# Performance work log

Hardware: AMD Instinct MI355X
Metric: run time of the kernel (lower is better)

## Reference

```python
import jax, jax.numpy as jnp
import numpy as np

N_NODES = 50000
N_EDGES = 800000
IN_DIM = 256
OUT_DIM = 32
NUM_HEADS = 8


def setup_inputs() -> dict:
    key = jax.random.key(0)
    ks = jax.random.split(key, 9)
    h = jax.random.normal(ks[0], (N_NODES, IN_DIM), dtype=jnp.float32)
    src = jax.random.randint(ks[1], (N_EDGES,), 0, N_NODES, dtype=jnp.int32)
    dst = jax.random.randint(ks[2], (N_EDGES,), 0, N_NODES, dtype=jnp.int32)
    s = 1.0 / np.sqrt(IN_DIM)
    W_lin = jax.random.uniform(ks[3], (IN_DIM, IN_DIM), jnp.float32, -s, s)
    b_lin = jax.random.uniform(ks[4], (IN_DIM,), jnp.float32, -s, s)
    # DGL GATConv fc: Linear(in_feats, out_feats*num_heads, bias=False)
    W_gat = jax.random.normal(ks[5], (IN_DIM, NUM_HEADS * OUT_DIM), dtype=jnp.float32) * s
    attn_l = jax.random.normal(ks[6], (NUM_HEADS, OUT_DIM), dtype=jnp.float32) * 0.1
    attn_r = jax.random.normal(ks[7], (NUM_HEADS, OUT_DIM), dtype=jnp.float32) * 0.1
    gat_bias = jnp.zeros((NUM_HEADS * OUT_DIM,), dtype=jnp.float32)
    return {"h": h, "src": src, "dst": dst, "W_lin": W_lin, "b_lin": b_lin,
            "W_gat": W_gat, "attn_l": attn_l, "attn_r": attn_r, "gat_bias": gat_bias}


def reference(h, src, dst, W_lin, b_lin, W_gat, attn_l, attn_r, gat_bias):
    N = h.shape[0]
    # pre-linear (nn.Linear(in_dim, in_dim))
    h = h @ W_lin + b_lin                                   # [N, in_dim]
    h_in = h
    # GATConv (eval mode: feat_drop/attn_drop are identity)
    feat = (h @ W_gat).reshape(N, NUM_HEADS, OUT_DIM)       # [N, H, D]
    el = jnp.sum(feat * attn_l, axis=-1)                    # [N, H]
    er = jnp.sum(feat * attn_r, axis=-1)                    # [N, H]
    e = jax.nn.leaky_relu(el[src] + er[dst], 0.2)           # [E, H]  (DGL slope 0.2)
    # edge softmax normalized over incoming edges of each dst node
    m = jax.ops.segment_max(e, dst, num_segments=N)         # [N, H]
    m = jnp.where(jnp.isfinite(m), m, 0.0)                  # guard empty segments
    e = jnp.exp(e - m[dst])                                 # [E, H]
    s = jax.ops.segment_sum(e, dst, num_segments=N)         # [N, H]
    a = e / s[dst]                                          # [E, H]
    # weighted neighbor aggregation
    msg = feat[src] * a[:, :, None]                         # [E, H, D]
    out = jax.ops.segment_sum(msg, dst, num_segments=N)     # [N, H, D]
    out = out.reshape(N, NUM_HEADS * OUT_DIM) + gat_bias
    # GATLayer activation: F.leaky_relu (default slope 0.01), then residual
    out = jax.nn.leaky_relu(out, 0.01)
    return h_in + out
```

## Files before the change

kernel.cpp:

```cpp
#include <hip/hip_runtime.h>
#include <math.h>

#define NN 50000
#define NE 800000
#define DIM 256
#define NH 8
#define HD 32
#define CAP 64
#define GEMM_GRID ((NN + 63) / 64)
#define SCAT_GRID ((NE / 4 + 255) / 256)

typedef __attribute__((ext_vector_type(8))) short bf16x8;
typedef __attribute__((ext_vector_type(4))) float f32x4;
typedef unsigned short u16;

__device__ __forceinline__ u16 f2bf(float f) {
    unsigned u = __float_as_uint(f);
    return (u16)((u + 0x7FFFu + ((u >> 16) & 1u)) >> 16);
}

__global__ __launch_bounds__(256) void k_pack_zero(
    const float* __restrict__ Wl, const float* __restrict__ Wg,
    u16* __restrict__ Bl, u16* __restrict__ Bg, int* __restrict__ deg)
{
    int b = blockIdx.x;
    if (b < 512) {
        const float* W = (b < 256) ? Wl : Wg;
        u16* Bp = (b < 256) ? Bl : Bg;
        int idx = (b & 255) * 256 + threadIdx.x;
        int j    = idx & 7;
        int lane = (idx >> 3) & 63;
        int ks   = (idx >> 9) & 7;
        int nf   = idx >> 12;
        int n = nf * 16 + (lane & 15);
        int k = ks * 32 + (lane >> 4) * 8 + j;
        Bp[idx] = f2bf(W[k * 256 + n]);
    } else {
        int i = (b - 512) * 256 + threadIdx.x;
        if (i < NN / 4)
            ((int4*)deg)[i] = (int4){0, 0, 0, 0};
    }
}

template<int AF32, int DO_ELER, int HAS_BIAS>
__device__ void gemm_body(int bid, const void* __restrict__ A,
    const u16* __restrict__ Bp, const float* __restrict__ bias,
    u16* __restrict__ Cb, const float* __restrict__ attn_l,
    const float* __restrict__ attn_r, float* __restrict__ el,
    float* __restrict__ er, int M, u16* Bs)
{
    const int t    = threadIdx.x;
    const int lane = t & 63;
    const int wid  = t >> 6;
    const int row0 = bid * 64 + wid * 16;
    const int arow = min(row0 + (lane & 15), M - 1);
    const int kgrp = lane >> 4;

    bf16x8 af[8];
    if (AF32) {
        const float* ap = (const float*)A + (size_t)arow * DIM + kgrp * 8;
        #pragma unroll
        for (int ks = 0; ks < 8; ++ks) {
            float4 x = *(const float4*)(ap + ks * 32);
            float4 y = *(const float4*)(ap + ks * 32 + 4);
            bf16x8 v;
            v[0] = (short)f2bf(x.x); v[1] = (short)f2bf(x.y);
            v[2] = (short)f2bf(x.z); v[3] = (short)f2bf(x.w);
            v[4] = (short)f2bf(y.x); v[5] = (short)f2bf(y.y);
            v[6] = (short)f2bf(y.z); v[7] = (short)f2bf(y.w);
            af[ks] = v;
        }
    } else {
        const u16* ap = (const u16*)A + (size_t)arow * DIM + kgrp * 8;
        #pragma unroll
        for (int ks = 0; ks < 8; ++ks)
            af[ks] = *(const bf16x8*)(ap + ks * 32);
    }

    const int crow0 = row0 + (lane >> 4) * 4;
    const int ccol  = lane & 15;

    uint4 v0, v1, v2, v3;
    {
        const uint4* p = (const uint4*)Bp + t;
        v0 = p[0]; v1 = p[256]; v2 = p[512]; v3 = p[768];
    }

    for (int c = 0; c < 8; ++c) {
        __syncthreads();
        {
            uint4* q = (uint4*)Bs + t;
            q[0] = v0; q[256] = v1; q[512] = v2; q[768] = v3;
        }
        if (c < 7) {
            const uint4* p = (const uint4*)(Bp + (size_t)(c + 1) * 8192) + t;
            v0 = p[0]; v1 = p[256]; v2 = p[512]; v3 = p[768];
        }
        __syncthreads();

        f32x4 acc0 = (f32x4){0.f, 0.f, 0.f, 0.f};
        f32x4 acc1 = (f32x4){0.f, 0.f, 0.f, 0.f};
        const u16* ls = Bs + lane * 8;
        #pragma unroll
        for (int ks = 0; ks < 8; ++ks) {
            bf16x8 b0 = *(const bf16x8*)(ls + (size_t)ks * 512);
            bf16x8 b1 = *(const bf16x8*)(ls + (size_t)(8 + ks) * 512);
            acc0 = __builtin_amdgcn_mfma_f32_16x16x32_bf16(af[ks], b0, acc0, 0, 0, 0);
            acc1 = __builtin_amdgcn_mfma_f32_16x16x32_bf16(af[ks], b1, acc1, 0, 0, 0);
        }

        {
            int col0 = c * 32 + ccol;
            int col1 = col0 + 16;
            float bv0 = HAS_BIAS ? bias[col0] : 0.f;
            float bv1 = HAS_BIAS ? bias[col1] : 0.f;
            #pragma unroll
            for (int r = 0; r < 4; ++r) {
                int row = crow0 + r;
                if (row < M) {
                    Cb[(size_t)row * DIM + col0] = f2bf(acc0[r] + bv0);
                    Cb[(size_t)row * DIM + col1] = f2bf(acc1[r] + bv1);
                }
            }
        }

        if (DO_ELER) {
            float al0 = attn_l[c * HD + ccol], al1 = attn_l[c * HD + ccol + 16];
            float ar0 = attn_r[c * HD + ccol], ar1 = attn_r[c * HD + ccol + 16];
            float ep[4], rp[4];
            #pragma unroll
            for (int r = 0; r < 4; ++r) {
                ep[r] = acc0[r] * al0 + acc1[r] * al1;
                rp[r] = acc0[r] * ar0 + acc1[r] * ar1;
            }
            #pragma unroll
            for (int off = 1; off < 16; off <<= 1) {
                #pragma unroll
                for (int r = 0; r < 4; ++r) {
                    ep[r] += __shfl_xor(ep[r], off, 64);
                    rp[r] += __shfl_xor(rp[r], off, 64);
                }
            }
            int rsel = ccol & 3;
            float ev = (rsel == 0) ? ep[0] : (rsel == 1) ? ep[1] : (rsel == 2) ? ep[2] : ep[3];
            float rv = (rsel == 0) ? rp[0] : (rsel == 1) ? rp[1] : (rsel == 2) ? rp[2] : rp[3];
            int row = crow0 + rsel;
            if (ccol < 4)      { if (row < M) el[(size_t)row * NH + c] = ev; }
            else if (ccol < 8) { if (row < M) er[(size_t)row * NH + c] = rv; }
        }
    }
}

__global__ __launch_bounds__(256) void k_gemm1_scatter(
    const float* __restrict__ h, const u16* __restrict__ Bp1,
    const float* __restrict__ b_lin, u16* __restrict__ h1b,
    const int* __restrict__ src, const int* __restrict__ dst,
    int* __restrict__ deg, int* __restrict__ csr_pad)
{
    __shared__ u16 Bs[8192];
    int bid = blockIdx.x;
    if (bid < GEMM_GRID) {
        gemm_body<1, 0, 1>(bid, h, Bp1, b_lin, h1b,
                           nullptr, nullptr, nullptr, nullptr, NN, Bs);
    } else {
        int e0 = ((bid - GEMM_GRID) * 256 + threadIdx.x) * 4;
        if (e0 >= NE) return;
        int4 sv = *(const int4*)(src + e0);
        int4 dv = *(const int4*)(dst + e0);
        int p;
        p = atomicAdd(&deg[dv.x], 1); if (p < CAP) csr_pad[dv.x * CAP + p] = sv.x;
        p = atomicAdd(&deg[dv.y], 1); if (p < CAP) csr_pad[dv.y * CAP + p] = sv.y;
        p = atomicAdd(&deg[dv.z], 1); if (p < CAP) csr_pad[dv.z * CAP + p] = sv.z;
        p = atomicAdd(&deg[dv.w], 1); if (p < CAP) csr_pad[dv.w * CAP + p] = sv.w;
    }
}

__global__ __launch_bounds__(256) void k_gemm2(
    const u16* __restrict__ h1b, const u16* __restrict__ Bp2,
    u16* __restrict__ featb, const float* __restrict__ attn_l,
    const float* __restrict__ attn_r, float* __restrict__ el,
    float* __restrict__ er)
{
    __shared__ u16 Bs[8192];
    gemm_body<0, 1, 0>(blockIdx.x, h1b, Bp2, nullptr, featb,
                       attn_l, attn_r, el, er, NN, Bs);
}

#define BODYR(j)                                                         \
    {                                                                    \
        int   s  = __shfl(s_l, base32 + j0 + (j), 64);                   \
        float wv = __shfl((j) < 4 ? w0 : w1,                             \
                          base32 + ((j) & 3) * 8 + myhead, 64);          \
        uint4 fv = *(const uint4*)(featb + (size_t)s * DIM + c);         \
        acc0 += __uint_as_float(fv.x << 16)         * wv;                \
        acc1 += __uint_as_float(fv.x & 0xFFFF0000u) * wv;                \
        acc2 += __uint_as_float(fv.y << 16)         * wv;                \
        acc3 += __uint_as_float(fv.y & 0xFFFF0000u) * wv;                \
        acc4 += __uint_as_float(fv.z << 16)         * wv;                \
        acc5 += __uint_as_float(fv.z & 0xFFFF0000u) * wv;                \
        acc6 += __uint_as_float(fv.w << 16)         * wv;                \
        acc7 += __uint_as_float(fv.w & 0xFFFF0000u) * wv;                \
        sw   += wv;                                                      \
    }

__global__ __launch_bounds__(256) void aggregate_hw(
    const int* __restrict__ deg, const int* __restrict__ csr_pad,
    const float* __restrict__ el, const float* __restrict__ er,
    const u16* __restrict__ featb, const u16* __restrict__ h1b,
    const float* __restrict__ bias, float* __restrict__ out)
{
    const int t      = threadIdx.x;
    const int hl     = t & 31;
    const int d      = blockIdx.x * 8 + (t >> 5);
    const int myhead = hl >> 2;
    const int c      = hl * 8;
    const int base32 = t & 32;
    const int cnt  = min(deg[d], CAP);
    const int* ebase = csr_pad + (size_t)d * CAP;
    const float er_p = er[(size_t)d * NH + (hl & 7)];

    float acc0 = 0.f, acc1 = 0.f, acc2 = 0.f, acc3 = 0.f;
    float acc4 = 0.f, acc5 = 0.f, acc6 = 0.f, acc7 = 0.f, sw = 0.f;

    for (int base = 0; base < cnt; base += 32) {
        const int nb = min(32, cnt - base);
        int s_l = (hl < nb) ? ebase[base + hl] : 0;
        for (int j0 = 0; j0 < nb; j0 += 8) {
            const int m = min(8, nb - j0);
            int e0 = min(j0 + (hl >> 3), nb - 1);
            int e1 = min(j0 + 4 + (hl >> 3), nb - 1);
            int se0 = __shfl(s_l, base32 + e0, 64);
            int se1 = __shfl(s_l, base32 + e1, 64);
            float x0 = el[(size_t)se0 * NH + (hl & 7)] + er_p;
            float x1 = el[(size_t)se1 * NH + (hl & 7)] + er_p;
            x0 = x0 > 0.f ? x0 : 0.2f * x0;
            x1 = x1 > 0.f ? x1 : 0.2f * x1;
            float w0 = __expf(x0);
            float w1 = __expf(x1);
            if (m == 8) {
                int ss[8];
                #pragma unroll
                for (int j = 0; j < 8; ++j) ss[j] = __shfl(s_l, base32 + j0 + j, 64);
                uint4 fv[8];
                #pragma unroll
                for (int j = 0; j < 8; ++j)
                    fv[j] = *(const uint4*)(featb + (size_t)ss[j] * DIM + c);
                __builtin_amdgcn_sched_barrier(0);
                #pragma unroll
                for (int j = 0; j < 8; ++j) {
                    float wv = __shfl(j < 4 ? w0 : w1,
                                      base32 + (j & 3) * 8 + myhead, 64);
                    acc0 += __uint_as_float(fv[j].x << 16)         * wv;
                    acc1 += __uint_as_float(fv[j].x & 0xFFFF0000u) * wv;
                    acc2 += __uint_as_float(fv[j].y << 16)         * wv;
                    acc3 += __uint_as_float(fv[j].y & 0xFFFF0000u) * wv;
                    acc4 += __uint_as_float(fv[j].z << 16)         * wv;
                    acc5 += __uint_as_float(fv[j].z & 0xFFFF0000u) * wv;
                    acc6 += __uint_as_float(fv[j].w << 16)         * wv;
                    acc7 += __uint_as_float(fv[j].w & 0xFFFF0000u) * wv;
                    sw   += wv;
                }
            } else {
                for (int j = 0; j < m; ++j) BODYR(j)
            }
        }
    }

    const float rs = (cnt > 0) ? 1.f / sw : 0.f;
    uint4  hv = *(const uint4*)(h1b + (size_t)d * DIM + c);
    float4 b0 = *(const float4*)(bias + c);
    float4 b1 = *(const float4*)(bias + c + 4);
    float r;
    float4 o0, o1;
    r = acc0 * rs + b0.x; r = r > 0.f ? r : 0.01f * r; o0.x = __uint_as_float(hv.x << 16)         + r;
    r = acc1 * rs + b0.y; r = r > 0.f ? r : 0.01f * r; o0.y = __uint_as_float(hv.x & 0xFFFF0000u) + r;
    r = acc2 * rs + b0.z; r = r > 0.f ? r : 0.01f * r; o0.z = __uint_as_float(hv.y << 16)         + r;
    r = acc3 * rs + b0.w; r = r > 0.f ? r : 0.01f * r; o0.w = __uint_as_float(hv.y & 0xFFFF0000u) + r;
    r = acc4 * rs + b1.x; r = r > 0.f ? r : 0.01f * r; o1.x = __uint_as_float(hv.z << 16)         + r;
    r = acc5 * rs + b1.y; r = r > 0.f ? r : 0.01f * r; o1.y = __uint_as_float(hv.z & 0xFFFF0000u) + r;
    r = acc6 * rs + b1.z; r = r > 0.f ? r : 0.01f * r; o1.z = __uint_as_float(hv.w << 16)         + r;
    r = acc7 * rs + b1.w; r = r > 0.f ? r : 0.01f * r; o1.w = __uint_as_float(hv.w & 0xFFFF0000u) + r;
    *(float4*)(out + (size_t)d * DIM + c)     = o0;
    *(float4*)(out + (size_t)d * DIM + c + 4) = o1;
}

extern "C" void kernel_launch(void* const* d_in, const int* in_sizes, int n_in,
                              void* d_out, int out_size, void* d_ws, size_t ws_size,
                              hipStream_t stream)
{
    const float* h      = (const float*)d_in[0];
    const int*   src    = (const int*)d_in[1];
    const int*   dst    = (const int*)d_in[2];
    const float* W_lin  = (const float*)d_in[3];
    const float* b_lin  = (const float*)d_in[4];
    const float* W_gat  = (const float*)d_in[5];
    const float* attn_l = (const float*)d_in[6];
    const float* attn_r = (const float*)d_in[7];
    const float* g_bias = (const float*)d_in[8];
    float* out = (float*)d_out;

    u16*   h1b    = (u16*)d_ws;
    u16*   featb  = h1b + (size_t)NN * DIM;
    u16*   Bp_lin = featb + (size_t)NN * DIM;
    u16*   Bp_gat = Bp_lin + 65536;
    float* el     = (float*)(Bp_gat + 65536);
    float* er     = el + (size_t)NN * NH;
    int*   deg     = (int*)(er + (size_t)NN * NH);
    int*   csr_pad = deg + NN + 8;

    k_pack_zero<<<512 + 64, 256, 0, stream>>>(W_lin, W_gat, Bp_lin, Bp_gat, deg);
    k_gemm1_scatter<<<GEMM_GRID + SCAT_GRID, 256, 0, stream>>>(
        h, Bp_lin, b_lin, h1b, src, dst, deg, csr_pad);
    k_gemm2<<<GEMM_GRID, 256, 0, stream>>>(h1b, Bp_gat, featb, attn_l, attn_r, el, er);
    aggregate_hw<<<NN / 8, 256, 0, stream>>>(deg, csr_pad, el, er, featb,
                                             h1b, g_bias, out);
}
```

Baseline: 171.0 us.

## Make GEMMs persistent with full weight matrix in LDS and split scatter across both

Both GEMM kernels become persistent 256-block launches that load the entire 256x256 bf16 weight matrix into 128KB of LDS once per block. Each wave then loops over 16-row tiles and computes all 256 output columns with 16 accumulators. The per-chunk barriers and repeated weight reloads go away. The CSR edge scatter now runs in two extra waves per block and is split between the two GEMM kernels, so the atomics overlap with matrix work. The cost is heavy LDS and register use, which caps occupancy at about one block per CU, and the code assumes NN is divisible by 16 because the row bounds checks are dropped.

```diff
diff --git a/kernel.cpp b/kernel.cpp
--- a/kernel.cpp
+++ b/kernel.cpp
@@ -7,8 +7,11 @@
 #define NH 8
 #define HD 32
 #define CAP 64
-#define GEMM_GRID ((NN + 63) / 64)
-#define SCAT_GRID ((NE / 4 + 255) / 256)
+#define NTILES (NN / 16)
+#define PG_GRID 256
+#define GW 8
+#define SW 2
+#define PG_THR ((GW + SW) * 64)
 
 typedef __attribute__((ext_vector_type(8))) short bf16x8;
 typedef __attribute__((ext_vector_type(4))) float f32x4;
@@ -43,130 +46,103 @@
 }
 
 template<int AF32, int DO_ELER, int HAS_BIAS>
-__device__ void gemm_body(int bid, const void* __restrict__ A,
-    const u16* __restrict__ Bp, const float* __restrict__ bias,
-    u16* __restrict__ Cb, const float* __restrict__ attn_l,
-    const float* __restrict__ attn_r, float* __restrict__ el,
-    float* __restrict__ er, int M, u16* Bs)
+__device__ void gemm_pers(const void* __restrict__ A, const u16* __restrict__ Bp,
+    const float* __restrict__ bias, u16* __restrict__ Cb,
+    const float* __restrict__ attn_l, const float* __restrict__ attn_r,
+    float* __restrict__ el, float* __restrict__ er, u16* Bs)
 {
     const int t    = threadIdx.x;
     const int lane = t & 63;
     const int wid  = t >> 6;
-    const int row0 = bid * 64 + wid * 16;
-    const int arow = min(row0 + (lane & 15), M - 1);
+    const int ccol = lane & 15;
     const int kgrp = lane >> 4;
-
-    bf16x8 af[8];
-    if (AF32) {
-        const float* ap = (const float*)A + (size_t)arow * DIM + kgrp * 8;
+    const u16* ls = Bs + lane * 8;
+
+    for (int tile = blockIdx.x * GW + wid; tile < NTILES; tile += PG_GRID * GW) {
+        const int row0 = tile * 16;
+        const int arow = row0 + ccol;
+
+        bf16x8 af[8];
+        if (AF32) {
+            const float* ap = (const float*)A + (size_t)arow * DIM + kgrp * 8;
+            #pragma unroll
+            for (int ks = 0; ks < 8; ++ks) {
+                float4 x = *(const float4*)(ap + ks * 32);
+                float4 y = *(const float4*)(ap + ks * 32 + 4);
+                bf16x8 v;
+                v[0] = (short)f2bf(x.x); v[1] = (short)f2bf(x.y);
+                v[2] = (short)f2bf(x.z); v[3] = (short)f2bf(x.w);
+                v[4] = (short)f2bf(y.x); v[5] = (short)f2bf(y.y);
+                v[6] = (short)f2bf(y.z); v[7] = (short)f2bf(y.w);
+                af[ks] = v;
+            }
+        } else {
+            const u16* ap = (const u16*)A + (size_t)arow * DIM + kgrp * 8;
+            #pragma unroll
+            for (int ks = 0; ks < 8; ++ks)
+                af[ks] = *(const bf16x8*)(ap + ks * 32);
+        }
+
+        f32x4 acc[16];
+        #pragma unroll
+        for (int i = 0; i < 16; ++i) acc[i] = (f32x4){0.f, 0.f, 0.f, 0.f};
         #pragma unroll
         for (int ks = 0; ks < 8; ++ks) {
-            float4 x = *(const float4*)(ap + ks * 32);
-            float4 y = *(const float4*)(ap + ks * 32 + 4);
-            bf16x8 v;
-            v[0] = (short)f2bf(x.x); v[1] = (short)f2bf(x.y);
-            v[2] = (short)f2bf(x.z); v[3] = (short)f2bf(x.w);
-            v[4] = (short)f2bf(y.x); v[5] = (short)f2bf(y.y);
-            v[6] = (short)f2bf(y.z); v[7] = (short)f2bf(y.w);
-            af[ks] = v;
-        }
-    } else {
-        const u16* ap = (const u16*)A + (size_t)arow * DIM + kgrp * 8;
-        #pragma unroll
-        for (int ks = 0; ks < 8; ++ks)
-            af[ks] = *(const bf16x8*)(ap + ks * 32);
-    }
-
-    const int crow0 = row0 + (lane >> 4) * 4;
-    const int ccol  = lane & 15;
-
-    uint4 v0, v1, v2, v3;
-    {
-        const uint4* p = (const uint4*)Bp + t;
-        v0 = p[0]; v1 = p[256]; v2 = p[512]; v3 = p[768];
-    }
-
-    for (int c = 0; c < 8; ++c) {
-        __syncthreads();
-        {
-            uint4* q = (uint4*)Bs + t;
-            q[0] = v0; q[256] = v1; q[512] = v2; q[768] = v3;
-        }
-        if (c < 7) {
-            const uint4* p = (const uint4*)(Bp + (size_t)(c + 1) * 8192) + t;
-            v0 = p[0]; v1 = p[256]; v2 = p[512]; v3 = p[768];
-        }
-        __syncthreads();
-
-        f32x4 acc0 = (f32x4){0.f, 0.f, 0.f, 0.f};
-        f32x4 acc1 = (f32x4){0.f, 0.f, 0.f, 0.f};
-        const u16* ls = Bs + lane * 8;
-        #pragma unroll
-        for (int ks = 0; ks < 8; ++ks) {
-            bf16x8 b0 = *(const bf16x8*)(ls + (size_t)ks * 512);
-            bf16x8 b1 = *(const bf16x8*)(ls + (size_t)(8 + ks) * 512);
-            acc0 = __builtin_amdgcn_mfma_f32_16x16x32_bf16(af[ks], b0, acc0, 0, 0, 0);
-            acc1 = __builtin_amdgcn_mfma_f32_16x16x32_bf16(af[ks], b1, acc1, 0, 0, 0);
-        }
-
-        {
-            int col0 = c * 32 + ccol;
-            int col1 = col0 + 16;
-            float bv0 = HAS_BIAS ? bias[col0] : 0.f;
-            float bv1 = HAS_BIAS ? bias[col1] : 0.f;
-            #pragma unroll
-            for (int r = 0; r < 4; ++r) {
-                int row = crow0 + r;
-                if (row < M) {
-                    Cb[(size_t)row * DIM + col0] = f2bf(acc0[r] + bv0);
-                    Cb[(size_t)row * DIM + col1] = f2bf(acc1[r] + bv1);
+            #pragma unroll
+            for (int nf = 0; nf < 16; ++nf) {
+                bf16x8 bfr = *(const bf16x8*)(ls + (size_t)(nf * 8 + ks) * 512);
+                acc[nf] = __builtin_amdgcn_mfma_f32_16x16x32_bf16(af[ks], bfr, acc[nf], 0, 0, 0);
+            }
+        }
+
+        const int crow0 = row0 + kgrp * 4;
+        #pragma unroll
+        for (int nf = 0; nf < 16; ++nf) {
+            int col = nf * 16 + ccol;
+            float bv = HAS_BIAS ? bias[col] : 0.f;
+            #pragma unroll
+            for (int r = 0; r < 4; ++r)
+                Cb[(size_t)(crow0 + r) * DIM + col] = f2bf(acc[nf][r] + bv);
+        }
+
+        if (DO_ELER) {
+            #pragma unroll
+            for (int hh = 0; hh < 8; ++hh) {
+                float al0 = attn_l[hh * HD + ccol], al1 = attn_l[hh * HD + 16 + ccol];
+                float ar0 = attn_r[hh * HD + ccol], ar1 = attn_r[hh * HD + 16 + ccol];
+                float ep[4], rp[4];
+                #pragma unroll
+                for (int r = 0; r < 4; ++r) {
+                    ep[r] = acc[2 * hh][r] * al0 + acc[2 * hh + 1][r] * al1;
+                    rp[r] = acc[2 * hh][r] * ar0 + acc[2 * hh + 1][r] * ar1;
                 }
+                #pragma unroll
+                for (int off = 1; off < 16; off <<= 1) {
+                    #pragma unroll
+                    for (int r = 0; r < 4; ++r) {
+                        ep[r] += __shfl_xor(ep[r], off, 64);
+                        rp[r] += __shfl_xor(rp[r], off, 64);
+                    }
+                }
+                int rsel = ccol & 3;
+                float ev = (rsel == 0) ? ep[0] : (rsel == 1) ? ep[1] : (rsel == 2) ? ep[2] : ep[3];
+                float rv = (rsel == 0) ? rp[0] : (rsel == 1) ? rp[1] : (rsel == 2) ? rp[2] : rp[3];
+                int row = crow0 + rsel;
+                if (ccol < 4)      el[(size_t)row * NH + hh] = ev;
+                else if (ccol < 8) er[(size_t)row * NH + hh] = rv;
             }
         }
-
-        if (DO_ELER) {
-            float al0 = attn_l[c * HD + ccol], al1 = attn_l[c * HD + ccol + 16];
-            float ar0 = attn_r[c * HD + ccol], ar1 = attn_r[c * HD + ccol + 16];
-            float ep[4], rp[4];
-            #pragma unroll
-            for (int r = 0; r < 4; ++r) {
-                ep[r] = acc0[r] * al0 + acc1[r] * al1;
-                rp[r] = acc0[r] * ar0 + acc1[r] * ar1;
-            }
-            #pragma unroll
-            for (int off = 1; off < 16; off <<= 1) {
-                #pragma unroll
-                for (int r = 0; r < 4; ++r) {
-                    ep[r] += __shfl_xor(ep[r], off, 64);
-                    rp[r] += __shfl_xor(rp[r], off, 64);
-                }
-            }
-            int rsel = ccol & 3;
-            float ev = (rsel == 0) ? ep[0] : (rsel == 1) ? ep[1] : (rsel == 2) ? ep[2] : ep[3];
-            float rv = (rsel == 0) ? rp[0] : (rsel == 1) ? rp[1] : (rsel == 2) ? rp[2] : rp[3];
-            int row = crow0 + rsel;
-            if (ccol < 4)      { if (row < M) el[(size_t)row * NH + c] = ev; }
-            else if (ccol < 8) { if (row < M) er[(size_t)row * NH + c] = rv; }
-        }
-    }
-}
-
-__global__ __launch_bounds__(256) void k_gemm1_scatter(
-    const float* __restrict__ h, const u16* __restrict__ Bp1,
-    const float* __restrict__ b_lin, u16* __restrict__ h1b,
+    }
+}
+
+__device__ __forceinline__ void scatter_waves(
     const int* __restrict__ src, const int* __restrict__ dst,
-    int* __restrict__ deg, int* __restrict__ csr_pad)
-{
-    __shared__ u16 Bs[8192];
-    int bid = blockIdx.x;
-    if (bid < GEMM_GRID) {
-        gemm_body<1, 0, 1>(bid, h, Bp1, b_lin, h1b,
-                           nullptr, nullptr, nullptr, nullptr, NN, Bs);
-    } else {
-        int e0 = ((bid - GEMM_GRID) * 256 + threadIdx.x) * 4;
-        if (e0 >= NE) return;
-        int4 sv = *(const int4*)(src + e0);
-        int4 dv = *(const int4*)(dst + e0);
+    int* __restrict__ deg, int* __restrict__ csr_pad, int g_lo, int g_hi)
+{
+    int sid = blockIdx.x * (SW * 64) + (threadIdx.x - GW * 64);
+    for (int g = g_lo + sid; g < g_hi; g += PG_GRID * SW * 64) {
+        int4 sv = *(const int4*)(src + g * 4);
+        int4 dv = *(const int4*)(dst + g * 4);
         int p;
         p = atomicAdd(&deg[dv.x], 1); if (p < CAP) csr_pad[dv.x * CAP + p] = sv.x;
         p = atomicAdd(&deg[dv.y], 1); if (p < CAP) csr_pad[dv.y * CAP + p] = sv.y;
@@ -175,15 +151,49 @@
     }
 }
 
-__global__ __launch_bounds__(256) void k_gemm2(
+__global__ __launch_bounds__(PG_THR) void k_gemm1_scatter(
+    const float* __restrict__ h, const u16* __restrict__ Bp1,
+    const float* __restrict__ b_lin, u16* __restrict__ h1b,
+    const int* __restrict__ src, const int* __restrict__ dst,
+    int* __restrict__ deg, int* __restrict__ csr_pad)
+{
+    extern __shared__ u16 Bs[];
+    const int t = threadIdx.x;
+    if (t < 512) {
+        const uint4* p = (const uint4*)Bp1;
+        uint4* q = (uint4*)Bs;
+        #pragma unroll
+        for (int i = 0; i < 16; ++i)
+            q[i * 512 + t] = p[i * 512 + t];
+    }
+    __syncthreads();
+    if ((t >> 6) < GW)
+        gemm_pers<1, 0, 1>(h, Bp1, b_lin, h1b, nullptr, nullptr, nullptr, nullptr, Bs);
+    else
+        scatter_waves(src, dst, deg, csr_pad, 0, NE / 8);
+}
+
+__global__ __launch_bounds__(PG_THR) void k_gemm2_scatter(
     const u16* __restrict__ h1b, const u16* __restrict__ Bp2,
     u16* __restrict__ featb, const float* __restrict__ attn_l,
     const float* __restrict__ attn_r, float* __restrict__ el,
-    float* __restrict__ er)
-{
-    __shared__ u16 Bs[8192];
-    gemm_body<0, 1, 0>(blockIdx.x, h1b, Bp2, nullptr, featb,
-                       attn_l, attn_r, el, er, NN, Bs);
+    float* __restrict__ er, const int* __restrict__ src,
+    const int* __restrict__ dst, int* __restrict__ deg, int* __restrict__ csr_pad)
+{
+    extern __shared__ u16 Bs[];
+    const int t = threadIdx.x;
+    if (t < 512) {
+        const uint4* p = (const uint4*)Bp2;
+        uint4* q = (uint4*)Bs;
+        #pragma unroll
+        for (int i = 0; i < 16; ++i)
+            q[i * 512 + t] = p[i * 512 + t];
+    }
+    __syncthreads();
+    if ((t >> 6) < GW)
+        gemm_pers<0, 1, 0>(h1b, Bp2, nullptr, featb, attn_l, attn_r, el, er, Bs);
+    else
+        scatter_waves(src, dst, deg, csr_pad, NE / 8, NE / 4);
 }
 
 #define BODYR(j)                                                         \
@@ -309,9 +319,10 @@
     int*   csr_pad = deg + NN + 8;
 
     k_pack_zero<<<512 + 64, 256, 0, stream>>>(W_lin, W_gat, Bp_lin, Bp_gat, deg);
-    k_gemm1_scatter<<<GEMM_GRID + SCAT_GRID, 256, 0, stream>>>(
+    k_gemm1_scatter<<<PG_GRID, PG_THR, 131072, stream>>>(
         h, Bp_lin, b_lin, h1b, src, dst, deg, csr_pad);
-    k_gemm2<<<GEMM_GRID, 256, 0, stream>>>(h1b, Bp_gat, featb, attn_l, attn_r, el, er);
+    k_gemm2_scatter<<<PG_GRID, PG_THR, 131072, stream>>>(
+        h1b, Bp_gat, featb, attn_l, attn_r, el, er, src, dst, deg, csr_pad);
     aggregate_hw<<<NN / 8, 256, 0, stream>>>(deg, csr_pad, el, er, featb,
                                              h1b, g_bias, out);
 }
```

Measured after the change: 332.5 us. 94.5% more time.
